# Performance work log

Hardware: AMD Instinct MI355X
Metric: run time of the kernel (lower is better)

The kernel has to match this reference:

```python
import math
import jax, jax.numpy as jnp
import numpy as np

D_MODEL = 1024
NHEAD = 16
HEAD_DIM = D_MODEL // NHEAD
BATCH = 2
SEQ = 2048


def setup_inputs() -> dict:
    key = jax.random.key(0)
    ks = jax.random.split(key, 8)
    data = jax.random.normal(ks[0], (BATCH, SEQ, D_MODEL), dtype=jnp.float32)
    temporal = jax.random.uniform(ks[1], (BATCH, SEQ), dtype=jnp.float32)
    mask = jnp.zeros((SEQ, SEQ), dtype=jnp.float32)
    s = 1.0 / math.sqrt(D_MODEL)
    Wq = jax.random.normal(ks[2], (D_MODEL, D_MODEL), dtype=jnp.float32) * s
    Wk = jax.random.normal(ks[3], (D_MODEL, D_MODEL), dtype=jnp.float32) * s
    Wv = jax.random.normal(ks[4], (D_MODEL, D_MODEL), dtype=jnp.float32) * s
    bq = jax.random.normal(ks[5], (D_MODEL,), dtype=jnp.float32) * 0.02
    bk = jax.random.normal(ks[6], (D_MODEL,), dtype=jnp.float32) * 0.02
    bv = jax.random.normal(ks[7], (D_MODEL,), dtype=jnp.float32) * 0.02
    return {"data": data, "temporal": temporal, "mask": mask,
            "Wq": Wq, "bq": bq, "Wk": Wk, "bk": bk, "Wv": Wv, "bv": bv}


def _rotate_half_pairs(x):
    # x: [..., s] with s even; pairs (x0,x1) -> (-x1, x0) interleaved
    x2 = x.reshape(x.shape[:-1] + (-1, 2))  # [..., s//2, 2]
    rot = jnp.stack([-x2[..., 1], x2[..., 0]], axis=-1)
    return rot.reshape(x.shape)


def reference(data, temporal, mask, Wq, bq, Wk, bk, Wv, bv):
    B, L, D = data.shape
    H, S = NHEAD, HEAD_DIM
    scale = math.sqrt(S)

    query = (data @ Wq + bq).reshape(B, L, H, S)
    key_ = (data @ Wk + bk).reshape(B, L, H, S)
    value = (data @ Wv + bv).reshape(B, L, H, S)

    # freq = 10000^(-arange(0, S, 2)/S), repeat_interleave(2) -> [S]
    freq = jnp.power(10000.0, -jnp.arange(0, S, 2, dtype=jnp.float32) / S)
    freq = jnp.repeat(freq, 2)
    freqs = temporal[:, :, None] * freq[None, None, :]  # [B, L, S]
    cosine = jnp.cos(freqs)[:, :, None, :]  # [B, L, 1, S]
    sine = jnp.sin(freqs)[:, :, None, :]

    rq = query * cosine + _rotate_half_pairs(query) * sine
    rk = key_ * cosine + _rotate_half_pairs(key_) * sine

    logits = jnp.einsum('bqhs,bkhs->bhqk', rq, rk) / scale
    logits = logits + mask  # mask: [L, L], broadcasts over b,h
    weights = jax.nn.softmax(logits, axis=-1)
    context = jnp.einsum('bhqk,bkhs->bqhs', weights, value)
    return context.reshape(B, L, D)
```

## Files before the change

kernel.cpp:

```cpp
#include <hip/hip_runtime.h>
#include <hip/hip_bf16.h>

#define D_MODEL 1024
#define NHEAD   16
#define HEAD_DIM 64
#define BATCH   2
#define SEQ     2048
#define NTOK    (BATCH*SEQ)

#define FREQ_LOG2 0.20762050593046015f

typedef short  bfrag __attribute__((ext_vector_type(8)));
typedef float  ffrag __attribute__((ext_vector_type(4)));

__device__ inline ushort f2bf(float x) {
    __hip_bfloat16 h = __float2bfloat16(x);
    return __builtin_bit_cast(ushort, h);
}
__device__ inline void split_bf(float x, ushort& hi, ushort& lo) {
    __hip_bfloat16 h = __float2bfloat16(x);
    hi = __builtin_bit_cast(ushort, h);
    lo = f2bf(x - __bfloat162float(h));
}

__device__ inline void gload16(const ushort* g, ushort* l) {
    __builtin_amdgcn_global_load_lds(
        (const __attribute__((address_space(1))) void*)g,
        (__attribute__((address_space(3))) void*)l, 16, 0, 0);
}

__global__ __launch_bounds__(256)
void split_data(const float* __restrict__ x, ushort* __restrict__ hi,
                ushort* __restrict__ lo)
{
    const int i4 = (blockIdx.x * 256 + threadIdx.x) * 4;
    const float4 v = *(const float4*)(x + i4);
    ushort4 h, l;
    split_bf(v.x, h.x, l.x); split_bf(v.y, h.y, l.y);
    split_bf(v.z, h.z, l.z); split_bf(v.w, h.w, l.w);
    *(ushort4*)(hi + i4) = h;
    *(ushort4*)(lo + i4) = l;
}

__global__ __launch_bounds__(256)
void split_tr_w(const float* __restrict__ Wq, const float* __restrict__ Wk,
                const float* __restrict__ Wv, ushort* __restrict__ hi)
{
    const int z = blockIdx.z;
    const float* W = (z == 0) ? Wq : (z == 1) ? Wk : Wv;
    ushort* thi = hi + (size_t)z * D_MODEL * D_MODEL;

    __shared__ float T[64][65];
    const int t  = threadIdx.x;
    const int k0 = blockIdx.x * 64, n0 = blockIdx.y * 64;

    #pragma unroll
    for (int i = 0; i < 4; i++) {
        const int f = i * 256 + t, r = f >> 4, c = (f & 15) * 4;
        const float4 v = *(const float4*)(W + (size_t)(k0 + r) * D_MODEL + n0 + c);
        T[r][c] = v.x; T[r][c + 1] = v.y; T[r][c + 2] = v.z; T[r][c + 3] = v.w;
    }
    __syncthreads();
    #pragma unroll
    for (int i = 0; i < 4; i++) {
        const int f = i * 256 + t, nr = f >> 4, kc = (f & 15) * 4;
        ushort4 h;
        h.x = f2bf(T[kc + 0][nr]);
        h.y = f2bf(T[kc + 1][nr]);
        h.z = f2bf(T[kc + 2][nr]);
        h.w = f2bf(T[kc + 3][nr]);
        const size_t o = (size_t)(n0 + nr) * D_MODEL + k0 + kc;
        *(ushort4*)(thi + o) = h;
    }
}

#define BK 32

union GemmSM {
    ushort st[2][3][128 * BK];
    float  c[64 * 132];
};

__global__ __launch_bounds__(256, 3)
void gemm_qkv(const ushort* __restrict__ Ahi, const ushort* __restrict__ Alo,
              const ushort* __restrict__ WThi,
              const float* __restrict__ bq, const float* __restrict__ bk,
              const float* __restrict__ bv, const float* __restrict__ temporal,
              ushort* __restrict__ Qhi, ushort* __restrict__ Qlo,
              ushort* __restrict__ Khi,
              ushort* __restrict__ VT)
{
    __shared__ GemmSM sm;
    const int z  = blockIdx.z;
    const int m0 = blockIdx.x * 128;
    const int n0 = blockIdx.y * 128;
    const float* bias = (z == 0) ? bq : (z == 1) ? bk : bv;
    const ushort* Bh = WThi + (size_t)z * D_MODEL * D_MODEL;

    const int t = threadIdx.x;
    const int w = t >> 6, lane = t & 63;
    const int lane15 = lane & 15, quad = lane >> 4, quad8 = quad * 8;
    const int wm = (w >> 1) * 64, wn = (w & 1) * 64;

    ffrag acc[4][4];
    #pragma unroll
    for (int i = 0; i < 4; i++)
        #pragma unroll
        for (int j = 0; j < 4; j++) acc[i][j] = (ffrag){0.f, 0.f, 0.f, 0.f};

    const int wr = w * 32;
    const int lr = lane >> 2;
    const int lc = (((lane & 3) ^ ((lane >> 3) & 3))) * 8;

    auto stage = [&](int bsel, int k0) {
        #pragma unroll
        for (int ch = 0; ch < 2; ch++) {
            const int rb = wr + ch * 16;
            const ushort* ga = Ahi + (size_t)(m0 + rb + lr) * D_MODEL + k0 + lc;
            const ushort* gl = Alo + (size_t)(m0 + rb + lr) * D_MODEL + k0 + lc;
            const ushort* gb = Bh  + (size_t)(n0 + rb + lr) * D_MODEL + k0 + lc;
            gload16(ga, &sm.st[bsel][0][rb * BK]);
            gload16(gl, &sm.st[bsel][1][rb * BK]);
            gload16(gb, &sm.st[bsel][2][rb * BK]);
        }
    };

    stage(0, 0);
    __syncthreads();

    const int rdsw = (quad ^ ((lane15 >> 1) & 3)) * 8;

    int buf = 0;
    for (int k0 = 0; k0 < D_MODEL; k0 += BK) {
        if (k0 + BK < D_MODEL) stage(buf ^ 1, k0 + BK);

        bfrag ah[4], al[4];
        #pragma unroll
        for (int mt = 0; mt < 4; mt++) {
            ah[mt] = *(const bfrag*)&sm.st[buf][0][(wm + mt * 16 + lane15) * BK + rdsw];
            al[mt] = *(const bfrag*)&sm.st[buf][1][(wm + mt * 16 + lane15) * BK + rdsw];
        }
        #pragma unroll
        for (int nt = 0; nt < 4; nt++) {
            const bfrag bh = *(const bfrag*)&sm.st[buf][2][(wn + nt * 16 + lane15) * BK + rdsw];
            #pragma unroll
            for (int mt = 0; mt < 4; mt++) {
                ffrag a = acc[mt][nt];
                a = __builtin_amdgcn_mfma_f32_16x16x32_bf16(ah[mt], bh, a, 0, 0, 0);
                a = __builtin_amdgcn_mfma_f32_16x16x32_bf16(al[mt], bh, a, 0, 0, 0);
                acc[mt][nt] = a;
            }
        }
        __syncthreads();
        buf ^= 1;
    }

    float bn[4];
    #pragma unroll
    for (int nt = 0; nt < 4; nt++) bn[nt] = bias[n0 + wn + nt * 16 + lane15];

    const int CST = (z == 2) ? 129 : 132;

    #pragma unroll
    for (int p = 0; p < 2; p++) {
        if (p) __syncthreads();
        if ((w >> 1) == p) {
            #pragma unroll
            for (int mt = 0; mt < 4; mt++)
                #pragma unroll
                for (int nt = 0; nt < 4; nt++)
                    #pragma unroll
                    for (int rr = 0; rr < 4; rr++)
                        sm.c[(mt * 16 + quad * 4 + rr) * CST + wn + nt * 16 + lane15] =
                            acc[mt][nt][rr] + bn[nt];
        }
        __syncthreads();

        if (z < 2) {
            ushort* ohi = (z == 0) ? Qhi : Khi;
            const float sc = (z == 0) ? 0.125f : 1.0f;
            #pragma unroll
            for (int i = 0; i < 8; i++) {
                const int f = i * 256 + t, r = f >> 5, c4 = (f & 31) * 4;
                float4 v = *(float4*)&sm.c[r * 132 + c4];
                const int m = m0 + p * 64 + r;
                const float tv = temporal[m];
                const float fr0 = exp2f(-(float)(c4 & 63) * FREQ_LOG2);
                const float fr1 = exp2f(-(float)((c4 + 2) & 63) * FREQ_LOG2);
                float s0, c0, s1, c1v;
                __sincosf(tv * fr0, &s0, &c0);
                __sincosf(tv * fr1, &s1, &c1v);
                const float y0 = (v.x * c0 - v.y * s0) * sc;
                const float y1 = (v.y * c0 + v.x * s0) * sc;
                const float y2 = (v.z * c1v - v.w * s1) * sc;
                const float y3 = (v.w * c1v + v.z * s1) * sc;
                ushort4 h, l;
                split_bf(y0, h.x, l.x); split_bf(y1, h.y, l.y);
                split_bf(y2, h.z, l.z); split_bf(y3, h.w, l.w);
                const size_t o = (size_t)m * D_MODEL + n0 + c4;
                *(ushort4*)(ohi + o) = h;
                if (z == 0) *(ushort4*)(Qlo + o) = l;
            }
        } else {
            const int bb = m0 >> 11;
            #pragma unroll
            for (int i = 0; i < 4; i++) {
                const int cid = i * 256 + t, col = cid >> 3, tg = (cid & 7) * 8;
                ushort u8[8];
                #pragma unroll
                for (int j = 0; j < 8; j++) u8[j] = f2bf(sm.c[(tg + j) * 129 + col]);
                const int ncol = n0 + col, hh = ncol >> 6, d = ncol & 63;
                const size_t dst = ((size_t)(bb * NHEAD + hh) * HEAD_DIM + d) * SEQ +
                                   (m0 & (SEQ - 1)) + p * 64 + tg;
                *(int4*)(VT + dst) = *(int4*)u8;
            }
        }
    }
}

#define KLD 72

__global__ __launch_bounds__(256, 4)
void attn_mfma(const ushort* __restrict__ Qhi, const ushort* __restrict__ Qlo,
               const ushort* __restrict__ Khi,
               const ushort* __restrict__ VT,  const float* __restrict__ mask,
               float* __restrict__ out)
{
    __shared__ ushort lsK[64 * KLD], lsV[64 * KLD], lsP[64 * KLD];

    const int bid  = blockIdx.x;
    const int bh   = (bid & 7) * 4 + (bid >> 8);
    const int qb   = (bid >> 3) & 31;
    const int b    = bh >> 4, h = bh & 15;
    const int q0   = qb * 64;

    const int t = threadIdx.x, w = t >> 6, lane = t & 63;
    const int lane15 = lane & 15, quad = lane >> 4, quad8 = quad * 8;
    const size_t tok0 = (size_t)b * SEQ;

    bfrag qh[2], ql[2];
    const size_t qrow = (tok0 + q0 + w * 16 + lane15) * D_MODEL + h * HEAD_DIM;
    #pragma unroll
    for (int ks = 0; ks < 2; ks++) {
        qh[ks] = *(const bfrag*)(Qhi + qrow + ks * 32 + quad8);
        ql[ks] = *(const bfrag*)(Qlo + qrow + ks * 32 + quad8);
    }

    ffrag of[4];
    #pragma unroll
    for (int nt = 0; nt < 4; nt++) of[nt] = (ffrag){0.f, 0.f, 0.f, 0.f};
    float l_i[4] = {0.f, 0.f, 0.f, 0.f};

    const int r1 = t >> 3,    c1 = (t & 7) * 8;
    const int r2 = 32 + r1,   c2 = c1;
    const ushort* Kh0 = Khi + tok0 * D_MODEL + h * HEAD_DIM;
    const ushort* Vt0 = VT + (size_t)(b * NHEAD + h) * HEAD_DIM * SEQ;

    int4 pk0 = *(const int4*)(Kh0 + (size_t)r1 * D_MODEL + c1);
    int4 pk1 = *(const int4*)(Kh0 + (size_t)r2 * D_MODEL + c2);
    int4 pv0 = *(const int4*)(Vt0 + (size_t)r1 * SEQ + c1);
    int4 pv1 = *(const int4*)(Vt0 + (size_t)r2 * SEQ + c2);

    const float* mrow = mask + (size_t)(q0 + w * 16 + quad * 4) * SEQ;

    for (int kt = 0; kt < SEQ; kt += 64) {
        *(int4*)&lsK[r1 * KLD + c1] = pk0;  *(int4*)&lsK[r2 * KLD + c2] = pk1;
        *(int4*)&lsV[r1 * KLD + c1] = pv0;  *(int4*)&lsV[r2 * KLD + c2] = pv1;
        __syncthreads();

        const int ktn = (kt + 64 < SEQ) ? kt + 64 : 0;
        pk0 = *(const int4*)(Kh0 + (size_t)(ktn + r1) * D_MODEL + c1);
        pk1 = *(const int4*)(Kh0 + (size_t)(ktn + r2) * D_MODEL + c2);
        pv0 = *(const int4*)(Vt0 + (size_t)r1 * SEQ + ktn + c1);
        pv1 = *(const int4*)(Vt0 + (size_t)r2 * SEQ + ktn + c2);

        float mv[4][4];
        #pragma unroll
        for (int nt = 0; nt < 4; nt++)
            #pragma unroll
            for (int rr = 0; rr < 4; rr++)
                mv[nt][rr] = mrow[(size_t)rr * SEQ + kt + nt * 16 + lane15];

        ffrag s[4];
        #pragma unroll
        for (int nt = 0; nt < 4; nt++) {
            ffrag a = (ffrag){0.f, 0.f, 0.f, 0.f};
            #pragma unroll
            for (int ks = 0; ks < 2; ks++) {
                const bfrag kf = *(const bfrag*)&lsK[(nt * 16 + lane15) * KLD + ks * 32 + quad8];
                a = __builtin_amdgcn_mfma_f32_16x16x32_bf16(qh[ks], kf, a, 0, 0, 0);
                a = __builtin_amdgcn_mfma_f32_16x16x32_bf16(ql[ks], kf, a, 0, 0, 0);
            }
            s[nt] = a;
        }

        #pragma unroll
        for (int nt = 0; nt < 4; nt++) {
            #pragma unroll
            for (int rr = 0; rr < 4; rr++) {
                const float e = __expf(s[nt][rr] + mv[nt][rr]);
                l_i[rr] += e;
                lsP[(w * 16 + quad * 4 + rr) * KLD + nt * 16 + lane15] = f2bf(e);
            }
        }

        #pragma unroll
        for (int ks = 0; ks < 2; ks++) {
            const bfrag pf = *(const bfrag*)&lsP[(w * 16 + lane15) * KLD + ks * 32 + quad8];
            #pragma unroll
            for (int nt = 0; nt < 4; nt++) {
                const bfrag vf = *(const bfrag*)&lsV[(nt * 16 + lane15) * KLD + ks * 32 + quad8];
                of[nt] = __builtin_amdgcn_mfma_f32_16x16x32_bf16(pf, vf, of[nt], 0, 0, 0);
            }
        }
        __syncthreads();
    }

    float inv[4];
    #pragma unroll
    for (int rr = 0; rr < 4; rr++) {
        float v = l_i[rr];
        #pragma unroll
        for (int off = 1; off < 16; off <<= 1) v += __shfl_xor(v, off);
        inv[rr] = 1.0f / v;
    }
    #pragma unroll
    for (int nt = 0; nt < 4; nt++)
        #pragma unroll
        for (int rr = 0; rr < 4; rr++)
            out[(tok0 + q0 + w * 16 + quad * 4 + rr) * D_MODEL + h * HEAD_DIM +
                nt * 16 + lane15] = of[nt][rr] * inv[rr];
}

extern "C" void kernel_launch(void* const* d_in, const int* in_sizes, int n_in,
                              void* d_out, int out_size, void* d_ws, size_t ws_size,
                              hipStream_t stream)
{
    const float* data     = (const float*)d_in[0];
    const float* temporal = (const float*)d_in[1];
    const float* mask     = (const float*)d_in[2];
    const float* Wq = (const float*)d_in[3];
    const float* bq = (const float*)d_in[4];
    const float* Wk = (const float*)d_in[5];
    const float* bk = (const float*)d_in[6];
    const float* Wv = (const float*)d_in[7];
    const float* bv = (const float*)d_in[8];
    float* out = (float*)d_out;

    char* ws = (char*)d_ws;
    const size_t MB = 1024 * 1024;
    ushort* Ahi  = (ushort*)(ws + 0 * MB);
    ushort* Alo  = (ushort*)(ws + 8 * MB);
    ushort* WThi = (ushort*)(ws + 16 * MB);
    ushort* Qhi  = (ushort*)(ws + 28 * MB);
    ushort* Qlo  = (ushort*)(ws + 36 * MB);
    ushort* Khi  = (ushort*)(ws + 44 * MB);
    ushort* VT   = (ushort*)(ws + 60 * MB);

    split_data<<<dim3(NTOK * D_MODEL / 1024), 256, 0, stream>>>(data, Ahi, Alo);
    split_tr_w<<<dim3(16, 16, 3), 256, 0, stream>>>(Wq, Wk, Wv, WThi);
    gemm_qkv<<<dim3(NTOK / 128, D_MODEL / 128, 3), 256, 0, stream>>>(
        Ahi, Alo, WThi, bq, bk, bv, temporal,
        Qhi, Qlo, Khi, VT);
    attn_mfma<<<dim3(BATCH * NHEAD * SEQ / 64), 256, 0, stream>>>(
        Qhi, Qlo, Khi, VT, mask, out);
}
```

Before: 268.7 us.

## Double-buffer K/V tiles in attention and swizzle LDS layouts instead of padding

The attention kernel now keeps two LDS buffers for K and V. The next tile is written into the alternate buffer while the current one is consumed, which removes one of the two barriers per iteration, and global prefetch now runs two tiles ahead. The padded row stride of 72 is replaced by an XOR swizzle on 8-element chunks for K, V and P to avoid bank conflicts without padding. This raises LDS use from about 27KB to 40KB per block, which may cut occupancy below the 4 blocks the launch bounds request, and makes the index arithmetic more complex.

```diff
diff --git a/kernel.cpp b/kernel.cpp
--- a/kernel.cpp
+++ b/kernel.cpp
@@ -99,7 +99,7 @@
 
     const int t = threadIdx.x;
     const int w = t >> 6, lane = t & 63;
-    const int lane15 = lane & 15, quad = lane >> 4, quad8 = quad * 8;
+    const int lane15 = lane & 15, quad8 = (lane >> 4) * 8, quad = lane >> 4;
     const int wm = (w >> 1) * 64, wn = (w & 1) * 64;
 
     ffrag acc[4][4];
@@ -218,15 +218,13 @@
     }
 }
 
-#define KLD 72
-
 __global__ __launch_bounds__(256, 4)
 void attn_mfma(const ushort* __restrict__ Qhi, const ushort* __restrict__ Qlo,
                const ushort* __restrict__ Khi,
                const ushort* __restrict__ VT,  const float* __restrict__ mask,
                float* __restrict__ out)
 {
-    __shared__ ushort lsK[64 * KLD], lsV[64 * KLD], lsP[64 * KLD];
+    __shared__ ushort lsK[2][64 * 64], lsV[2][64 * 64], lsP[64 * 64];
 
     const int bid  = blockIdx.x;
     const int bh   = (bid & 7) * 4 + (bid >> 8);
@@ -235,15 +233,15 @@
     const int q0   = qb * 64;
 
     const int t = threadIdx.x, w = t >> 6, lane = t & 63;
-    const int lane15 = lane & 15, quad = lane >> 4, quad8 = quad * 8;
+    const int lane15 = lane & 15, quad = lane >> 4;
     const size_t tok0 = (size_t)b * SEQ;
 
     bfrag qh[2], ql[2];
     const size_t qrow = (tok0 + q0 + w * 16 + lane15) * D_MODEL + h * HEAD_DIM;
     #pragma unroll
     for (int ks = 0; ks < 2; ks++) {
-        qh[ks] = *(const bfrag*)(Qhi + qrow + ks * 32 + quad8);
-        ql[ks] = *(const bfrag*)(Qlo + qrow + ks * 32 + quad8);
+        qh[ks] = *(const bfrag*)(Qhi + qrow + ks * 32 + quad * 8);
+        ql[ks] = *(const bfrag*)(Qlo + qrow + ks * 32 + quad * 8);
     }
 
     ffrag of[4];
@@ -251,28 +249,40 @@
     for (int nt = 0; nt < 4; nt++) of[nt] = (ffrag){0.f, 0.f, 0.f, 0.f};
     float l_i[4] = {0.f, 0.f, 0.f, 0.f};
 
-    const int r1 = t >> 3,    c1 = (t & 7) * 8;
-    const int r2 = 32 + r1,   c2 = c1;
+    const int r1 = t >> 3,  c1 = (t & 7) * 8;
+    const int sw = ((t & 7) ^ (r1 & 7)) * 8;
     const ushort* Kh0 = Khi + tok0 * D_MODEL + h * HEAD_DIM;
     const ushort* Vt0 = VT + (size_t)(b * NHEAD + h) * HEAD_DIM * SEQ;
 
     int4 pk0 = *(const int4*)(Kh0 + (size_t)r1 * D_MODEL + c1);
-    int4 pk1 = *(const int4*)(Kh0 + (size_t)r2 * D_MODEL + c2);
+    int4 pk1 = *(const int4*)(Kh0 + (size_t)(32 + r1) * D_MODEL + c1);
     int4 pv0 = *(const int4*)(Vt0 + (size_t)r1 * SEQ + c1);
-    int4 pv1 = *(const int4*)(Vt0 + (size_t)r2 * SEQ + c2);
+    int4 pv1 = *(const int4*)(Vt0 + (size_t)(32 + r1) * SEQ + c1);
+
+    *(int4*)&lsK[0][r1 * 64 + sw]        = pk0;
+    *(int4*)&lsK[0][(32 + r1) * 64 + sw] = pk1;
+    *(int4*)&lsV[0][r1 * 64 + sw]        = pv0;
+    *(int4*)&lsV[0][(32 + r1) * 64 + sw] = pv1;
+
+    pk0 = *(const int4*)(Kh0 + (size_t)(64 + r1) * D_MODEL + c1);
+    pk1 = *(const int4*)(Kh0 + (size_t)(96 + r1) * D_MODEL + c1);
+    pv0 = *(const int4*)(Vt0 + (size_t)r1 * SEQ + 64 + c1);
+    pv1 = *(const int4*)(Vt0 + (size_t)(32 + r1) * SEQ + 64 + c1);
+    __syncthreads();
 
     const float* mrow = mask + (size_t)(q0 + w * 16 + quad * 4) * SEQ;
 
+    const int krd = lane15 & 7;
+    const int keyr = (((lane15 >> 2) & 3) << 1) | (lane15 & 1);
+
+    int cur = 0;
     for (int kt = 0; kt < SEQ; kt += 64) {
-        *(int4*)&lsK[r1 * KLD + c1] = pk0;  *(int4*)&lsK[r2 * KLD + c2] = pk1;
-        *(int4*)&lsV[r1 * KLD + c1] = pv0;  *(int4*)&lsV[r2 * KLD + c2] = pv1;
-        __syncthreads();
-
-        const int ktn = (kt + 64 < SEQ) ? kt + 64 : 0;
-        pk0 = *(const int4*)(Kh0 + (size_t)(ktn + r1) * D_MODEL + c1);
-        pk1 = *(const int4*)(Kh0 + (size_t)(ktn + r2) * D_MODEL + c2);
-        pv0 = *(const int4*)(Vt0 + (size_t)r1 * SEQ + ktn + c1);
-        pv1 = *(const int4*)(Vt0 + (size_t)r2 * SEQ + ktn + c2);
+        if (kt + 64 < SEQ) {
+            *(int4*)&lsK[cur ^ 1][r1 * 64 + sw]        = pk0;
+            *(int4*)&lsK[cur ^ 1][(32 + r1) * 64 + sw] = pk1;
+            *(int4*)&lsV[cur ^ 1][r1 * 64 + sw]        = pv0;
+            *(int4*)&lsV[cur ^ 1][(32 + r1) * 64 + sw] = pv1;
+        }
 
         float mv[4][4];
         #pragma unroll
@@ -281,13 +291,20 @@
             for (int rr = 0; rr < 4; rr++)
                 mv[nt][rr] = mrow[(size_t)rr * SEQ + kt + nt * 16 + lane15];
 
+        const int ktn = (kt + 128 < SEQ) ? kt + 128 : 0;
+        pk0 = *(const int4*)(Kh0 + (size_t)(ktn + r1) * D_MODEL + c1);
+        pk1 = *(const int4*)(Kh0 + (size_t)(ktn + 32 + r1) * D_MODEL + c1);
+        pv0 = *(const int4*)(Vt0 + (size_t)r1 * SEQ + ktn + c1);
+        pv1 = *(const int4*)(Vt0 + (size_t)(32 + r1) * SEQ + ktn + c1);
+
         ffrag s[4];
         #pragma unroll
         for (int nt = 0; nt < 4; nt++) {
             ffrag a = (ffrag){0.f, 0.f, 0.f, 0.f};
             #pragma unroll
             for (int ks = 0; ks < 2; ks++) {
-                const bfrag kf = *(const bfrag*)&lsK[(nt * 16 + lane15) * KLD + ks * 32 + quad8];
+                const bfrag kf = *(const bfrag*)&lsK[cur][(nt * 16 + lane15) * 64 +
+                                                          ((ks * 4 + quad) ^ krd) * 8];
                 a = __builtin_amdgcn_mfma_f32_16x16x32_bf16(qh[ks], kf, a, 0, 0, 0);
                 a = __builtin_amdgcn_mfma_f32_16x16x32_bf16(ql[ks], kf, a, 0, 0, 0);
             }
@@ -300,20 +317,26 @@
             for (int rr = 0; rr < 4; rr++) {
                 const float e = __expf(s[nt][rr] + mv[nt][rr]);
                 l_i[rr] += e;
-                lsP[(w * 16 + quad * 4 + rr) * KLD + nt * 16 + lane15] = f2bf(e);
+                const int prow = w * 16 + quad * 4 + rr;
+                const int pchk = (2 * nt + (lane15 >> 3)) ^ ((quad << 1) | (rr & 1));
+                lsP[prow * 64 + pchk * 8 + (lane15 & 7)] = f2bf(e);
             }
         }
 
         #pragma unroll
         for (int ks = 0; ks < 2; ks++) {
-            const bfrag pf = *(const bfrag*)&lsP[(w * 16 + lane15) * KLD + ks * 32 + quad8];
+            const bfrag pf = *(const bfrag*)&lsP[(w * 16 + lane15) * 64 +
+                                                 ((ks * 4 + quad) ^ keyr) * 8];
             #pragma unroll
             for (int nt = 0; nt < 4; nt++) {
-                const bfrag vf = *(const bfrag*)&lsV[(nt * 16 + lane15) * KLD + ks * 32 + quad8];
+                const bfrag vf = *(const bfrag*)&lsV[cur][(nt * 16 + lane15) * 64 +
+                                                          ((ks * 4 + quad) ^ krd) * 8];
                 of[nt] = __builtin_amdgcn_mfma_f32_16x16x32_bf16(pf, vf, of[nt], 0, 0, 0);
             }
         }
+
         __syncthreads();
+        cur ^= 1;
     }
 
     float inv[4];
```

Result: faster. 262.8 us (-2.2%).
